# Kernel tuning notes

Hardware: AMD Instinct MI355X
Metric: run time of the kernel (lower is better)

Reference implementation:

```python
import jax, jax.numpy as jnp
import numpy as np

N, E = 50000, 800000
F_IN, EDGE_DIM, H, C = 128, 64, 8, 32
NEG_SLOPE = 0.2


def setup_inputs() -> dict:
    key = jax.random.key(0)
    ks = jax.random.split(key, 9)
    return {
        "x": jax.random.normal(ks[0], (N, F_IN), dtype=jnp.float32),
        "edge_index": jax.random.randint(ks[1], (2, E), 0, N, dtype=jnp.int32),
        "edge_attr": jax.random.normal(ks[2], (E, EDGE_DIM), dtype=jnp.float32),
        "W": jax.random.normal(ks[3], (F_IN, H * C), dtype=jnp.float32) * 0.05,
        "att_src": jax.random.normal(ks[4], (H, C), dtype=jnp.float32) * 0.05,
        "att_dst": jax.random.normal(ks[5], (H, C), dtype=jnp.float32) * 0.05,
        "W_edge": jax.random.normal(ks[6], (EDGE_DIM, H * C), dtype=jnp.float32) * 0.05,
        "att_edge": jax.random.normal(ks[7], (H, C), dtype=jnp.float32) * 0.05,
        "bias": jax.random.normal(ks[8], (H * C,), dtype=jnp.float32) * 0.05,
    }


def reference(x, edge_index, edge_attr, W, att_src, att_dst, W_edge, att_edge, bias):
    src, dst = edge_index[0], edge_index[1]  # messages flow src -> dst
    # Pre-activation ReLU from Graph_intra.forward
    xr = jax.nn.relu(x)
    # Linear projection, per-head view: [N, H, C]
    xs = (xr @ W).reshape(N, H, C)
    # Per-node attention logits: [N, H]
    a_src = jnp.einsum("nhc,hc->nh", xs, att_src)
    a_dst = jnp.einsum("nhc,hc->nh", xs, att_dst)
    # Edge-feature attention contribution: [E, H]
    e_proj = (edge_attr @ W_edge).reshape(E, H, C)
    a_edge = jnp.einsum("ehc,hc->eh", e_proj, att_edge)
    # Per-edge logits + LeakyReLU
    alpha = jax.nn.leaky_relu(a_src[src] + a_dst[dst] + a_edge, NEG_SLOPE)  # [E, H]
    # Segment softmax over destination neighborhoods
    seg_max = jax.ops.segment_max(alpha, dst, num_segments=N)
    seg_max = jnp.where(jnp.isfinite(seg_max), seg_max, 0.0)
    alpha = jnp.exp(alpha - seg_max[dst])
    seg_sum = jax.ops.segment_sum(alpha, dst, num_segments=N)
    alpha = alpha / (seg_sum[dst] + 1e-16)
    # Weighted message aggregation: scatter-add alpha_e * x_src[e]
    msgs = alpha[:, :, None] * xs[src]  # [E, H, C]
    out = jax.ops.segment_sum(msgs, dst, num_segments=N)  # [N, H, C]
    return out.reshape(N, H * C) + bias
```

## Files before the change

kernel.cpp:

```cpp
#include <hip/hip_runtime.h>

#define N_NODES 50000
#define E_EDGES 800000
#define F_IN    128
#define EDGE_DIM 64
#define HC      256
#define NEG_SLOPE 0.2f

typedef __attribute__((ext_vector_type(8))) short short8;
typedef __attribute__((ext_vector_type(4))) float f32x4;

__device__ __forceinline__ unsigned short f2bf(float f) {
    unsigned u = __builtin_bit_cast(unsigned, f);
    u += 0x7fffu + ((u >> 16) & 1u);
    return (unsigned short)(u >> 16);
}
__device__ __forceinline__ float bf2f(unsigned short b) {
    return __builtin_bit_cast(float, (unsigned)b << 16);
}

__global__ __launch_bounds__(256) void k_pre(const float* __restrict__ W,
        const float* __restrict__ att_src, const float* __restrict__ att_dst,
        const float* __restrict__ W_edge, const float* __restrict__ att_edge,
        unsigned short* __restrict__ W_T, unsigned short* __restrict__ WaT,
        unsigned short* __restrict__ WaE, int* __restrict__ counts, int* __restrict__ gcur) {
    int idx = blockIdx.x * 256 + threadIdx.x;
    if (idx < N_NODES) counts[idx] = 0;
    if (idx == 0) *gcur = 0;
    if (idx < 32768) {
        int n = idx >> 7, k = idx & 127;
        W_T[n * 128 + k] = f2bf(W[k * 256 + n]);
    }
    if (idx < 2048) {
        int col = idx & 15, k = idx >> 4;
        const float* att = (col < 8) ? att_src : att_dst;
        int h = col & 7;
        float s = 0.f;
        #pragma unroll
        for (int c = 0; c < 32; ++c)
            s = fmaf(W[k * 256 + h * 32 + c], att[h * 32 + c], s);
        WaT[col * 128 + k] = f2bf(s);
    }
    if (idx < 1024) {
        int c = idx >> 6, k = idx & 63;
        float s = 0.f;
        if (c < 8) {
            #pragma unroll
            for (int cc = 0; cc < 32; ++cc)
                s = fmaf(W_edge[k * 256 + c * 32 + cc], att_edge[c * 32 + cc], s);
        }
        WaE[c * 64 + k] = (c < 8) ? f2bf(s) : (unsigned short)0;
    }
}

#define NT_TILES 782
#define GEMM_BLOCKS 512
#define HIST_BLOCKS 782
#define ALOG_BLOCKS 782
__global__ __launch_bounds__(256) void kBig(const float* __restrict__ x,
        const unsigned short* __restrict__ W_T, const unsigned short* __restrict__ WaT,
        const int4* __restrict__ dst4, int* __restrict__ counts, int4* __restrict__ slot4,
        unsigned short* __restrict__ xs, float* __restrict__ a_src, float* __restrict__ a_dst) {
    __shared__ __align__(16) unsigned short sB[128 * 128];
    int t = threadIdx.x;

    if (blockIdx.x >= GEMM_BLOCKS) {
        int part = blockIdx.x - GEMM_BLOCKS;
        if (part < HIST_BLOCKS) {
            int i = part * 256 + t;
            if (i < E_EDGES / 4) {
                int4 d = dst4[i];
                int4 sl;
                sl.x = atomicAdd(&counts[d.x], 1);
                sl.y = atomicAdd(&counts[d.y], 1);
                sl.z = atomicAdd(&counts[d.z], 1);
                sl.w = atomicAdd(&counts[d.w], 1);
                slot4[i] = sl;
            }
            return;
        }
        int tile = (part - HIST_BLOCKS) * 4 + (t >> 6);
        if (tile >= N_NODES / 16) return;
        int lane = t & 63, mr = lane & 15, g = lane >> 4;
        int node = tile * 16 + mr;
        f32x4 acc = (f32x4){0.f, 0.f, 0.f, 0.f};
        #pragma unroll
        for (int ks = 0; ks < 4; ++ks) {
            const float* xp = &x[(size_t)node * 128 + ks * 32 + g * 8];
            short8 a;
            #pragma unroll
            for (int j = 0; j < 8; ++j) a[j] = (short)f2bf(fmaxf(xp[j], 0.f));
            short8 b = *(const short8*)&WaT[mr * 128 + ks * 32 + g * 8];
            acc = __builtin_amdgcn_mfma_f32_16x16x32_bf16(a, b, acc, 0, 0, 0);
        }
        #pragma unroll
        for (int r = 0; r < 4; ++r) {
            int n2 = tile * 16 + g * 4 + r;
            if (mr < 8) a_src[n2 * 8 + mr]       = acc[r];
            else        a_dst[n2 * 8 + (mr - 8)] = acc[r];
        }
        return;
    }

    int ch = blockIdx.x >> 8;
    int rt0 = blockIdx.x & 255;
    for (int G = t; G < 2048; G += 256) {
        int nn = G >> 4, gi = G & 15;
        *(int4*)&sB[(nn * 16 + (gi ^ (nn & 7))) * 8] =
            *(const int4*)&W_T[(ch * 128 + nn) * 128 + gi * 8];
    }
    __syncthreads();
    int lane = t & 63, w = t >> 6, mr = lane & 15, g = lane >> 4;

    for (int rt = rt0; rt < NT_TILES; rt += 256) {
        int node = rt * 64 + w * 16 + mr;
        short8 a[4];
        if (node < N_NODES) {
            #pragma unroll
            for (int ks = 0; ks < 4; ++ks) {
                const float* xp = &x[(size_t)node * 128 + ks * 32 + g * 8];
                #pragma unroll
                for (int j = 0; j < 8; ++j) a[ks][j] = (short)f2bf(fmaxf(xp[j], 0.f));
            }
        } else {
            #pragma unroll
            for (int ks = 0; ks < 4; ++ks)
                #pragma unroll
                for (int j = 0; j < 8; ++j) a[ks][j] = 0;
        }

        f32x4 acc[8];
        #pragma unroll
        for (int i = 0; i < 8; ++i) acc[i] = (f32x4){0.f, 0.f, 0.f, 0.f};

        #pragma unroll
        for (int ks = 0; ks < 4; ++ks) {
            int posk = (ks * 4 + g) ^ (mr & 7);
            #pragma unroll
            for (int nt = 0; nt < 8; ++nt) {
                short8 b = *(const short8*)&sB[((nt * 16 + mr) * 16 + posk) * 8];
                acc[nt] = __builtin_amdgcn_mfma_f32_16x16x32_bf16(a[ks], b, acc[nt], 0, 0, 0);
            }
        }

        #pragma unroll
        for (int r = 0; r < 4; ++r) {
            int node2 = rt * 64 + w * 16 + g * 4 + r;
            if (node2 < N_NODES) {
                #pragma unroll
                for (int nt = 0; nt < 8; ++nt)
                    xs[(size_t)node2 * 256 + ch * 128 + nt * 16 + mr] = f2bf(acc[nt][r]);
            }
        }
    }
}

__global__ __launch_bounds__(256) void kB_alloc(const int* __restrict__ counts,
                                                int* __restrict__ starts,
                                                int* __restrict__ gcur) {
    int n = blockIdx.x * 256 + threadIdx.x;
    int c = (n < N_NODES) ? counts[n] : 0;
    int incl = c;
    #pragma unroll
    for (int off = 1; off < 64; off <<= 1) {
        int u = __shfl_up(incl, off);
        if ((threadIdx.x & 63) >= off) incl += u;
    }
    int total = __shfl(incl, 63);
    int wavebase = 0;
    if ((threadIdx.x & 63) == 63) wavebase = atomicAdd(gcur, total);
    wavebase = __shfl(wavebase, 63);
    if (n < N_NODES) starts[n] = wavebase + incl - c;
}

__global__ __launch_bounds__(256) void kEdge(const float* __restrict__ ea,
        const unsigned short* __restrict__ WaE,
        const int* __restrict__ src, const int* __restrict__ dst,
        const int* __restrict__ slot, const int* __restrict__ starts,
        const float* __restrict__ a_src, const float* __restrict__ a_dst,
        _Float16* __restrict__ w_perm, int* __restrict__ src_perm) {
    __shared__ int s_sn[256], s_dn[256], s_pos[256];
    __shared__ _Float16 s_w[256 * 8];
    int t = threadIdx.x;
    int blockbase = blockIdx.x * 256;
    {
        int e = blockbase + t;
        int dn = dst[e], sn = src[e];
        int pos = starts[dn] + slot[e];
        s_sn[t] = sn; s_dn[t] = dn; s_pos[t] = pos;
        src_perm[pos] = sn;
    }
    __syncthreads();
    int lane = t & 63, w = t >> 6;
    int mr = lane & 15, g = lane >> 4;
    short8 b0 = *(const short8*)&WaE[mr * 64 + g * 8];
    short8 b1 = *(const short8*)&WaE[mr * 64 + 32 + g * 8];
    #pragma unroll
    for (int ti = 0; ti < 4; ++ti) {
        int lb = w * 64 + ti * 16;
        int er = blockbase + lb + mr;
        const float* ap = &ea[(size_t)er * 64 + g * 8];
        short8 a0, a1;
        #pragma unroll
        for (int j = 0; j < 8; ++j) a0[j] = (short)f2bf(ap[j]);
        #pragma unroll
        for (int j = 0; j < 8; ++j) a1[j] = (short)f2bf(ap[32 + j]);
        f32x4 acc = (f32x4){0.f, 0.f, 0.f, 0.f};
        acc = __builtin_amdgcn_mfma_f32_16x16x32_bf16(a0, b0, acc, 0, 0, 0);
        acc = __builtin_amdgcn_mfma_f32_16x16x32_bf16(a1, b1, acc, 0, 0, 0);
        if (mr < 8) {
            #pragma unroll
            for (int r = 0; r < 4; ++r) {
                int le = lb + g * 4 + r;
                int sn = s_sn[le], dn = s_dn[le];
                float v = acc[r] + a_src[sn * 8 + mr] + a_dst[dn * 8 + mr];
                v = (v > 0.f) ? v : NEG_SLOPE * v;
                s_w[le * 8 + mr] = (_Float16)__expf(v);
            }
        }
    }
    __syncthreads();
    *(int4*)&w_perm[(size_t)s_pos[t] * 8] = *(const int4*)&s_w[t * 8];
}

__global__ __launch_bounds__(256) void k6_wave(
    const int* __restrict__ starts, const int* __restrict__ counts,
    const _Float16* __restrict__ w_perm, const int* __restrict__ src_perm,
    const unsigned short* __restrict__ xs, const float* __restrict__ bias,
    float* __restrict__ out) {
    int lane = threadIdx.x & 63;
    int n = blockIdx.x * 4 + (threadIdx.x >> 6);
    if (n >= N_NODES) return;
    int start = starts[n], cnt = counts[n];
    int j = lane >> 3;
    int l5 = lane & 31;
    int h2 = lane >> 5;
    int hq = l5 >> 2;

    float acc[8];
    #pragma unroll
    for (int k = 0; k < 8; ++k) acc[k] = 0.f;
    float psum = 0.f;

    for (int base = 0; base < cnt; base += 8) {
        int nk = cnt - base; if (nk > 8) nk = 8;
        float wv = (float)w_perm[(size_t)(start + base) * 8 + lane];
        if (j >= nk) wv = 0.f;
        psum += wv;
        int sv = src_perm[start + base + (lane & 7)];
        #pragma unroll
        for (int jj = 0; jj < 8; jj += 2) {
            int eidx = jj + h2;
            int s = __shfl(sv, eidx);
            s = (eidx < nk) ? s : 0;
            float w = __shfl(wv, eidx * 8 + hq);
            int4 xv = *(const int4*)&xs[(size_t)s * 256 + l5 * 8];
            acc[0] = fmaf(w, bf2f((unsigned short)(xv.x & 0xffff)), acc[0]);
            acc[1] = fmaf(w, bf2f((unsigned short)((unsigned)xv.x >> 16)), acc[1]);
            acc[2] = fmaf(w, bf2f((unsigned short)(xv.y & 0xffff)), acc[2]);
            acc[3] = fmaf(w, bf2f((unsigned short)((unsigned)xv.y >> 16)), acc[3]);
            acc[4] = fmaf(w, bf2f((unsigned short)(xv.z & 0xffff)), acc[4]);
            acc[5] = fmaf(w, bf2f((unsigned short)((unsigned)xv.z >> 16)), acc[5]);
            acc[6] = fmaf(w, bf2f((unsigned short)(xv.w & 0xffff)), acc[6]);
            acc[7] = fmaf(w, bf2f((unsigned short)((unsigned)xv.w >> 16)), acc[7]);
        }
    }
    #pragma unroll
    for (int k = 0; k < 8; ++k) acc[k] += __shfl_xor(acc[k], 32);
    psum += __shfl_xor(psum, 8);
    psum += __shfl_xor(psum, 16);
    psum += __shfl_xor(psum, 32);
    float denom = __shfl(psum, hq);
    float rinv = 1.0f / (denom + 1e-16f);

    if (h2 == 0) {
        const float* bp = &bias[l5 * 8];
        f32x4 o0, o1;
        #pragma unroll
        for (int k = 0; k < 4; ++k) o0[k] = acc[k] * rinv + bp[k];
        #pragma unroll
        for (int k = 0; k < 4; ++k) o1[k] = acc[4 + k] * rinv + bp[4 + k];
        float* op = &out[(size_t)n * 256 + l5 * 8];
        __builtin_nontemporal_store(o0, (f32x4*)op);
        __builtin_nontemporal_store(o1, (f32x4*)(op + 4));
    }
}

extern "C" void kernel_launch(void* const* d_in, const int* in_sizes, int n_in,
                              void* d_out, int out_size, void* d_ws, size_t ws_size,
                              hipStream_t stream) {
    const float* x         = (const float*)d_in[0];
    const int*   ei        = (const int*)d_in[1];
    const float* edge_attr = (const float*)d_in[2];
    const float* W         = (const float*)d_in[3];
    const float* att_src   = (const float*)d_in[4];
    const float* att_dst   = (const float*)d_in[5];
    const float* W_edge    = (const float*)d_in[6];
    const float* att_edge  = (const float*)d_in[7];
    const float* bias      = (const float*)d_in[8];
    float* out = (float*)d_out;

    const int* e_src = ei;
    const int* e_dst = ei + E_EDGES;

    char* p = (char*)d_ws;
    unsigned short* xs = (unsigned short*)p; p += (size_t)N_NODES * HC * 2;
    float* a_src   = (float*)p; p += (size_t)N_NODES * 8 * 4;
    float* a_dst   = (float*)p; p += (size_t)N_NODES * 8 * 4;
    _Float16* w_perm = (_Float16*)p; p += (size_t)E_EDGES * 8 * 2 + 256;
    int* src_perm  = (int*)p;   p += (size_t)E_EDGES * 4 + 256;
    int* slot      = (int*)p;   p += (size_t)E_EDGES * 4 + 256;
    unsigned short* W_T  = (unsigned short*)p; p += 32768 * 2;
    unsigned short* WaT  = (unsigned short*)p; p += 2048 * 2;
    unsigned short* WaE  = (unsigned short*)p; p += 1024 * 2;
    int* counts    = (int*)p;   p += 200192;
    int* starts    = (int*)p;   p += 200192;
    int* gcur      = (int*)p;   p += 256;

    hipLaunchKernelGGL(k_pre, dim3(196), dim3(256), 0, stream,
                       W, att_src, att_dst, W_edge, att_edge, W_T, WaT, WaE, counts, gcur);
    hipLaunchKernelGGL(kBig, dim3(GEMM_BLOCKS + HIST_BLOCKS + ALOG_BLOCKS), dim3(256), 0, stream,
                       x, W_T, WaT, (const int4*)e_dst, counts, (int4*)slot, xs, a_src, a_dst);
    hipLaunchKernelGGL(kB_alloc, dim3(196), dim3(256), 0, stream,
                       counts, starts, gcur);
    hipLaunchKernelGGL(kEdge, dim3(E_EDGES / 256), dim3(256), 0, stream,
                       edge_attr, WaE, e_src, e_dst, slot, starts,
                       a_src, a_dst, w_perm, src_perm);
    hipLaunchKernelGGL(k6_wave, dim3(N_NODES / 4), dim3(256), 0, stream,
                       starts, counts, w_perm, src_perm, xs, bias, out);
}
```

Baseline: 210.2 us.

## Split edge/aggregate phases by node halves and fuse attention logits into GEMM

Computes per-node attention logits inside the main GEMM blocks instead of separate blocks. Replaces the wave-level atomic scan with a single-block deterministic scan and adds a kernel that writes CSR-ordered edge records. Edge logits are then computed in CSR order, split at node 25000, so aggregation of the first half overlaps the edge work of the second half inside a fused kernel. The trade-offs are a serial single-block scan, 16-byte records per edge, extra launches, and gathered reads of edge_attr.

```diff
diff --git a/kernel.cpp b/kernel.cpp
--- a/kernel.cpp
+++ b/kernel.cpp
@@ -6,6 +6,7 @@
 #define EDGE_DIM 64
 #define HC      256
 #define NEG_SLOPE 0.2f
+#define SPLIT_NODE 25000
 
 typedef __attribute__((ext_vector_type(8))) short short8;
 typedef __attribute__((ext_vector_type(4))) float f32x4;
@@ -23,10 +24,9 @@
         const float* __restrict__ att_src, const float* __restrict__ att_dst,
         const float* __restrict__ W_edge, const float* __restrict__ att_edge,
         unsigned short* __restrict__ W_T, unsigned short* __restrict__ WaT,
-        unsigned short* __restrict__ WaE, int* __restrict__ counts, int* __restrict__ gcur) {
+        unsigned short* __restrict__ WaE, int* __restrict__ counts) {
     int idx = blockIdx.x * 256 + threadIdx.x;
     if (idx < N_NODES) counts[idx] = 0;
-    if (idx == 0) *gcur = 0;
     if (idx < 32768) {
         int n = idx >> 7, k = idx & 127;
         W_T[n * 128 + k] = f2bf(W[k * 256 + n]);
@@ -56,7 +56,6 @@
 #define NT_TILES 782
 #define GEMM_BLOCKS 512
 #define HIST_BLOCKS 782
-#define ALOG_BLOCKS 782
 __global__ __launch_bounds__(256) void kBig(const float* __restrict__ x,
         const unsigned short* __restrict__ W_T, const unsigned short* __restrict__ WaT,
         const int4* __restrict__ dst4, int* __restrict__ counts, int4* __restrict__ slot4,
@@ -65,39 +64,15 @@
     int t = threadIdx.x;
 
     if (blockIdx.x >= GEMM_BLOCKS) {
-        int part = blockIdx.x - GEMM_BLOCKS;
-        if (part < HIST_BLOCKS) {
-            int i = part * 256 + t;
-            if (i < E_EDGES / 4) {
-                int4 d = dst4[i];
-                int4 sl;
-                sl.x = atomicAdd(&counts[d.x], 1);
-                sl.y = atomicAdd(&counts[d.y], 1);
-                sl.z = atomicAdd(&counts[d.z], 1);
-                sl.w = atomicAdd(&counts[d.w], 1);
-                slot4[i] = sl;
-            }
-            return;
-        }
-        int tile = (part - HIST_BLOCKS) * 4 + (t >> 6);
-        if (tile >= N_NODES / 16) return;
-        int lane = t & 63, mr = lane & 15, g = lane >> 4;
-        int node = tile * 16 + mr;
-        f32x4 acc = (f32x4){0.f, 0.f, 0.f, 0.f};
-        #pragma unroll
-        for (int ks = 0; ks < 4; ++ks) {
-            const float* xp = &x[(size_t)node * 128 + ks * 32 + g * 8];
-            short8 a;
-            #pragma unroll
-            for (int j = 0; j < 8; ++j) a[j] = (short)f2bf(fmaxf(xp[j], 0.f));
-            short8 b = *(const short8*)&WaT[mr * 128 + ks * 32 + g * 8];
-            acc = __builtin_amdgcn_mfma_f32_16x16x32_bf16(a, b, acc, 0, 0, 0);
-        }
-        #pragma unroll
-        for (int r = 0; r < 4; ++r) {
-            int n2 = tile * 16 + g * 4 + r;
-            if (mr < 8) a_src[n2 * 8 + mr]       = acc[r];
-            else        a_dst[n2 * 8 + (mr - 8)] = acc[r];
+        int i = (blockIdx.x - GEMM_BLOCKS) * 256 + t;
+        if (i < E_EDGES / 4) {
+            int4 d = dst4[i];
+            int4 sl;
+            sl.x = atomicAdd(&counts[d.x], 1);
+            sl.y = atomicAdd(&counts[d.y], 1);
+            sl.z = atomicAdd(&counts[d.z], 1);
+            sl.w = atomicAdd(&counts[d.w], 1);
+            slot4[i] = sl;
         }
         return;
     }
@@ -111,6 +86,12 @@
     }
     __syncthreads();
     int lane = t & 63, w = t >> 6, mr = lane & 15, g = lane >> 4;
+    short8 wa[4];
+    if (ch == 0) {
+        #pragma unroll
+        for (int ks = 0; ks < 4; ++ks)
+            wa[ks] = *(const short8*)&WaT[mr * 128 + ks * 32 + g * 8];
+    }
 
     for (int rt = rt0; rt < NT_TILES; rt += 256) {
         int node = rt * 64 + w * 16 + mr;
@@ -132,6 +113,7 @@
         f32x4 acc[8];
         #pragma unroll
         for (int i = 0; i < 8; ++i) acc[i] = (f32x4){0.f, 0.f, 0.f, 0.f};
+        f32x4 acc17 = (f32x4){0.f, 0.f, 0.f, 0.f};
 
         #pragma unroll
         for (int ks = 0; ks < 4; ++ks) {
@@ -141,6 +123,8 @@
                 short8 b = *(const short8*)&sB[((nt * 16 + mr) * 16 + posk) * 8];
                 acc[nt] = __builtin_amdgcn_mfma_f32_16x16x32_bf16(a[ks], b, acc[nt], 0, 0, 0);
             }
+            if (ch == 0)
+                acc17 = __builtin_amdgcn_mfma_f32_16x16x32_bf16(a[ks], wa[ks], acc17, 0, 0, 0);
         }
 
         #pragma unroll
@@ -150,46 +134,62 @@
                 #pragma unroll
                 for (int nt = 0; nt < 8; ++nt)
                     xs[(size_t)node2 * 256 + ch * 128 + nt * 16 + mr] = f2bf(acc[nt][r]);
+                if (ch == 0) {
+                    if (mr < 8) a_src[node2 * 8 + mr]       = acc17[r];
+                    else        a_dst[node2 * 8 + (mr - 8)] = acc17[r];
+                }
             }
         }
     }
 }
 
-__global__ __launch_bounds__(256) void kB_alloc(const int* __restrict__ counts,
-                                                int* __restrict__ starts,
-                                                int* __restrict__ gcur) {
-    int n = blockIdx.x * 256 + threadIdx.x;
-    int c = (n < N_NODES) ? counts[n] : 0;
-    int incl = c;
+__global__ __launch_bounds__(1024) void kB_scan(const int* __restrict__ counts,
+                                                int* __restrict__ starts) {
+    __shared__ int sums[1024];
+    int t = threadIdx.x;
+    const int chunk = (N_NODES + 1023) / 1024;
+    int begin = t * chunk;
+    int end = begin + chunk; if (end > N_NODES) end = N_NODES;
+    int s = 0;
+    for (int i = begin; i < end && i < N_NODES; ++i) s += counts[i];
+    sums[t] = s;
+    __syncthreads();
+    for (int off = 1; off < 1024; off <<= 1) {
+        int tmp = (t >= off) ? sums[t - off] : 0;
+        __syncthreads();
+        sums[t] += tmp;
+        __syncthreads();
+    }
+    int base = sums[t] - s;
+    for (int i = begin; i < end && i < N_NODES; ++i) {
+        starts[i] = base;
+        base += counts[i];
+    }
+}
+
+__global__ __launch_bounds__(256) void kB2(const int* __restrict__ dst,
+        const int* __restrict__ slot, const int* __restrict__ starts,
+        const int* __restrict__ src, int4* __restrict__ rec4) {
+    int e = blockIdx.x * 1024 + threadIdx.x;
     #pragma unroll
-    for (int off = 1; off < 64; off <<= 1) {
-        int u = __shfl_up(incl, off);
-        if ((threadIdx.x & 63) >= off) incl += u;
-    }
-    int total = __shfl(incl, 63);
-    int wavebase = 0;
-    if ((threadIdx.x & 63) == 63) wavebase = atomicAdd(gcur, total);
-    wavebase = __shfl(wavebase, 63);
-    if (n < N_NODES) starts[n] = wavebase + incl - c;
-}
-
-__global__ __launch_bounds__(256) void kEdge(const float* __restrict__ ea,
+    for (int i = 0; i < 4; ++i, e += 256) {
+        if (e < E_EDGES) {
+            int p = starts[dst[e]] + slot[e];
+            rec4[p] = make_int4(e, src[e], dst[e], 0);
+        }
+    }
+}
+
+__device__ __forceinline__ void edge_tile(int tilebase, int plo, int phi,
+        const int4* __restrict__ rec4, const float* __restrict__ ea,
         const unsigned short* __restrict__ WaE,
-        const int* __restrict__ src, const int* __restrict__ dst,
-        const int* __restrict__ slot, const int* __restrict__ starts,
         const float* __restrict__ a_src, const float* __restrict__ a_dst,
-        _Float16* __restrict__ w_perm, int* __restrict__ src_perm) {
-    __shared__ int s_sn[256], s_dn[256], s_pos[256];
-    __shared__ _Float16 s_w[256 * 8];
-    int t = threadIdx.x;
-    int blockbase = blockIdx.x * 256;
-    {
-        int e = blockbase + t;
-        int dn = dst[e], sn = src[e];
-        int pos = starts[dn] + slot[e];
-        s_sn[t] = sn; s_dn[t] = dn; s_pos[t] = pos;
-        src_perm[pos] = sn;
-    }
+        _Float16* __restrict__ w_perm, int t,
+        int* s_e, int* s_sn, int* s_dn, _Float16* s_w) {
+    int p = tilebase + t;
+    int pc = (p < E_EDGES) ? p : (E_EDGES - 1);
+    int4 rv = rec4[pc];
+    s_e[t] = rv.x; s_sn[t] = rv.y; s_dn[t] = rv.z;
     __syncthreads();
     int lane = t & 63, w = t >> 6;
     int mr = lane & 15, g = lane >> 4;
@@ -198,8 +198,8 @@
     #pragma unroll
     for (int ti = 0; ti < 4; ++ti) {
         int lb = w * 64 + ti * 16;
-        int er = blockbase + lb + mr;
-        const float* ap = &ea[(size_t)er * 64 + g * 8];
+        int e = s_e[lb + mr];
+        const float* ap = &ea[(size_t)e * 64 + g * 8];
         short8 a0, a1;
         #pragma unroll
         for (int j = 0; j < 8; ++j) a0[j] = (short)f2bf(ap[j]);
@@ -220,17 +220,35 @@
         }
     }
     __syncthreads();
-    *(int4*)&w_perm[(size_t)s_pos[t] * 8] = *(const int4*)&s_w[t * 8];
-}
-
-__global__ __launch_bounds__(256) void k6_wave(
-    const int* __restrict__ starts, const int* __restrict__ counts,
-    const _Float16* __restrict__ w_perm, const int* __restrict__ src_perm,
-    const unsigned short* __restrict__ xs, const float* __restrict__ bias,
-    float* __restrict__ out) {
-    int lane = threadIdx.x & 63;
-    int n = blockIdx.x * 4 + (threadIdx.x >> 6);
-    if (n >= N_NODES) return;
+    if (p >= plo && p < phi)
+        *(int4*)&w_perm[(size_t)p * 8] = *(const int4*)&s_w[t * 8];
+}
+
+#define EDGE_GRID 1600
+__global__ __launch_bounds__(256) void kEdgeA(const float* __restrict__ ea,
+        const unsigned short* __restrict__ WaE, const int4* __restrict__ rec4,
+        const int* __restrict__ starts,
+        const float* __restrict__ a_src, const float* __restrict__ a_dst,
+        _Float16* __restrict__ w_perm) {
+    __shared__ int s_e[256], s_sn[256], s_dn[256];
+    __shared__ _Float16 s_w[256 * 8];
+    int bound = starts[SPLIT_NODE];
+    int ntile = (bound + 255) >> 8;
+    bool first = true;
+    for (int tp = blockIdx.x; tp < ntile; tp += EDGE_GRID) {
+        if (!first) __syncthreads();
+        first = false;
+        edge_tile(tp * 256, 0, bound, rec4, ea, WaE, a_src, a_dst, w_perm,
+                  threadIdx.x, s_e, s_sn, s_dn, s_w);
+    }
+}
+
+__device__ __forceinline__ void k6_body(int n, int t,
+        const int* __restrict__ starts, const int* __restrict__ counts,
+        const _Float16* __restrict__ w_perm, const int4* __restrict__ rec4,
+        const unsigned short* __restrict__ xs, const float* __restrict__ bias,
+        float* __restrict__ out) {
+    int lane = t & 63;
     int start = starts[n], cnt = counts[n];
     int j = lane >> 3;
     int l5 = lane & 31;
@@ -247,7 +265,7 @@
         float wv = (float)w_perm[(size_t)(start + base) * 8 + lane];
         if (j >= nk) wv = 0.f;
         psum += wv;
-        int sv = src_perm[start + base + (lane & 7)];
+        int sv = rec4[start + base + (lane & 7)].y;
         #pragma unroll
         for (int jj = 0; jj < 8; jj += 2) {
             int eidx = jj + h2;
@@ -286,6 +304,45 @@
     }
 }
 
+#define K6A_BLOCKS 6250
+__global__ __launch_bounds__(256) void kFuse(const float* __restrict__ ea,
+        const unsigned short* __restrict__ WaE, const int4* __restrict__ rec4,
+        const int* __restrict__ starts, const int* __restrict__ counts,
+        const float* __restrict__ a_src, const float* __restrict__ a_dst,
+        _Float16* __restrict__ w_perm,
+        const unsigned short* __restrict__ xs, const float* __restrict__ bias,
+        float* __restrict__ out) {
+    __shared__ int s_e[256], s_sn[256], s_dn[256];
+    __shared__ _Float16 s_w[256 * 8];
+    int t = threadIdx.x;
+    if (blockIdx.x < EDGE_GRID) {
+        int bound = starts[SPLIT_NODE];
+        int tp0 = bound >> 8;
+        const int ntile = E_EDGES / 256;
+        bool first = true;
+        for (int tp = tp0 + blockIdx.x; tp < ntile; tp += EDGE_GRID) {
+            if (!first) __syncthreads();
+            first = false;
+            edge_tile(tp * 256, bound, E_EDGES, rec4, ea, WaE, a_src, a_dst, w_perm,
+                      t, s_e, s_sn, s_dn, s_w);
+        }
+        return;
+    }
+    int n = (blockIdx.x - EDGE_GRID) * 4 + (t >> 6);
+    if (n >= SPLIT_NODE) return;
+    k6_body(n, t, starts, counts, w_perm, rec4, xs, bias, out);
+}
+
+__global__ __launch_bounds__(256) void k6B(
+        const int* __restrict__ starts, const int* __restrict__ counts,
+        const _Float16* __restrict__ w_perm, const int4* __restrict__ rec4,
+        const unsigned short* __restrict__ xs, const float* __restrict__ bias,
+        float* __restrict__ out) {
+    int n = SPLIT_NODE + blockIdx.x * 4 + (threadIdx.x >> 6);
+    if (n >= N_NODES) return;
+    k6_body(n, threadIdx.x, starts, counts, w_perm, rec4, xs, bias, out);
+}
+
 extern "C" void kernel_launch(void* const* d_in, const int* in_sizes, int n_in,
                               void* d_out, int out_size, void* d_ws, size_t ws_size,
                               hipStream_t stream) {
@@ -308,24 +365,26 @@
     float* a_src   = (float*)p; p += (size_t)N_NODES * 8 * 4;
     float* a_dst   = (float*)p; p += (size_t)N_NODES * 8 * 4;
     _Float16* w_perm = (_Float16*)p; p += (size_t)E_EDGES * 8 * 2 + 256;
-    int* src_perm  = (int*)p;   p += (size_t)E_EDGES * 4 + 256;
+    int4* rec4     = (int4*)p;  p += (size_t)E_EDGES * 16 + 256;
     int* slot      = (int*)p;   p += (size_t)E_EDGES * 4 + 256;
     unsigned short* W_T  = (unsigned short*)p; p += 32768 * 2;
     unsigned short* WaT  = (unsigned short*)p; p += 2048 * 2;
     unsigned short* WaE  = (unsigned short*)p; p += 1024 * 2;
     int* counts    = (int*)p;   p += 200192;
     int* starts    = (int*)p;   p += 200192;
-    int* gcur      = (int*)p;   p += 256;
 
     hipLaunchKernelGGL(k_pre, dim3(196), dim3(256), 0, stream,
-                       W, att_src, att_dst, W_edge, att_edge, W_T, WaT, WaE, counts, gcur);
-    hipLaunchKernelGGL(kBig, dim3(GEMM_BLOCKS + HIST_BLOCKS + ALOG_BLOCKS), dim3(256), 0, stream,
+                       W, att_src, att_dst, W_edge, att_edge, W_T, WaT, WaE, counts);
+    hipLaunchKernelGGL(kBig, dim3(GEMM_BLOCKS + HIST_BLOCKS), dim3(256), 0, stream,
                        x, W_T, WaT, (const int4*)e_dst, counts, (int4*)slot, xs, a_src, a_dst);
-    hipLaunchKernelGGL(kB_alloc, dim3(196), dim3(256), 0, stream,
-                       counts, starts, gcur);
-    hipLaunchKernelGGL(kEdge, dim3(E_EDGES / 256), dim3(256), 0, stream,
-                       edge_attr, WaE, e_src, e_dst, slot, starts,
-                       a_src, a_dst, w_perm, src_perm);
-    hipLaunchKernelGGL(k6_wave, dim3(N_NODES / 4), dim3(256), 0, stream,
-                       starts, counts, w_perm, src_perm, xs, bias, out);
-}
+    hipLaunchKernelGGL(kB_scan, dim3(1), dim3(1024), 0, stream, counts, starts);
+    hipLaunchKernelGGL(kB2, dim3((E_EDGES + 1023) / 1024), dim3(256), 0, stream,
+                       e_dst, slot, starts, e_src, rec4);
+    hipLaunchKernelGGL(kEdgeA, dim3(EDGE_GRID), dim3(256), 0, stream,
+                       edge_attr, WaE, rec4, starts, a_src, a_dst, w_perm);
+    hipLaunchKernelGGL(kFuse, dim3(EDGE_GRID + K6A_BLOCKS), dim3(256), 0, stream,
+                       edge_attr, WaE, rec4, starts, counts, a_src, a_dst, w_perm,
+                       xs, bias, out);
+    hipLaunchKernelGGL(k6B, dim3(K6A_BLOCKS), dim3(256), 0, stream,
+                       starts, counts, w_perm, rec4, xs, bias, out);
+}
```

New measurement: 272.7 us. +29.7%, slower.
